# Kernel optimization log

Hardware: AMD Instinct MI355X
Metric: run time of the kernel (lower is better)

## Reference

```python
import jax, jax.numpy as jnp
import numpy as np

N, M, FEAT, GROUP, EMB = 512, 4096, 1024, 16, 64
DIM_GROUP = FEAT // GROUP  # 64


def _make_boxes(key, n):
    k1, k2, k3, k4 = jax.random.split(key, 4)
    cx = jax.random.uniform(k1, (n,), minval=0.0, maxval=800.0)
    cy = jax.random.uniform(k2, (n,), minval=0.0, maxval=800.0)
    w = jax.random.uniform(k3, (n,), minval=16.0, maxval=256.0)
    h = jax.random.uniform(k4, (n,), minval=16.0, maxval=256.0)
    return jnp.stack([cx - 0.5 * w, cy - 0.5 * h, cx + 0.5 * w, cy + 0.5 * h], axis=1)


def setup_inputs() -> dict:
    key = jax.random.key(0)
    ks = jax.random.split(key, 10)
    return {
        "roi_feat": jax.random.normal(ks[0], (N, FEAT), dtype=jnp.float32),
        "ref_feat": jax.random.normal(ks[1], (M, FEAT), dtype=jnp.float32),
        "rois_cur": _make_boxes(ks[2], N),
        "rois_ref": _make_boxes(ks[3], M),
        "Wg_w": jax.random.normal(ks[4], (GROUP, EMB), dtype=jnp.float32) * 0.01,
        "Wg_b": jnp.zeros((GROUP,), dtype=jnp.float32),
        "Wq_w": jax.random.normal(ks[5], (FEAT, FEAT), dtype=jnp.float32) * (1.0 / np.sqrt(FEAT)),
        "Wq_b": jnp.zeros((FEAT,), dtype=jnp.float32),
        "Wk_w": jax.random.normal(ks[6], (FEAT, FEAT), dtype=jnp.float32) * (1.0 / np.sqrt(FEAT)),
        "Wk_b": jnp.zeros((FEAT,), dtype=jnp.float32),
        "Wv_w": jax.random.normal(ks[7], (FEAT, FEAT), dtype=jnp.float32) * 0.01,  # grouped 1x1 conv: [16 groups x 64 out, 1024 in-per-group]
        "Wv_b": jnp.zeros((FEAT,), dtype=jnp.float32),
    }


def _position_embedding(bbox, ref_bbox):
    # extract_position_matrix
    xmin, ymin, xmax, ymax = [ref_bbox[:, i] for i in range(4)]
    w_ref = xmax - xmin + 1.0
    h_ref = ymax - ymin + 1.0
    cx_ref = 0.5 * (xmin + xmax)
    cy_ref = 0.5 * (ymin + ymax)
    xmin, ymin, xmax, ymax = [bbox[:, i] for i in range(4)]
    w = xmax - xmin + 1.0
    h = ymax - ymin + 1.0
    cx = 0.5 * (xmin + xmax)
    cy = 0.5 * (ymin + ymax)
    dx = jnp.log(jnp.abs((cx[:, None] - cx_ref[None, :]) / w[:, None]) + 0.001)
    dy = jnp.log(jnp.abs((cy[:, None] - cy_ref[None, :]) / h[:, None]) + 0.001)
    dw = jnp.log(w[:, None] / w_ref[None, :])
    dh = jnp.log(h[:, None] / h_ref[None, :])
    pos = jnp.stack([dx, dy, dw, dh], axis=2)  # [N, M, 4]
    # extract_position_embedding with feat_dim=64, wave_length=1000
    feat_range = jnp.arange(EMB // 8, dtype=jnp.float32)  # 8
    dim_mat = jnp.power(1000.0, (8.0 / EMB) * feat_range)  # [8]
    div = (pos * 100.0)[..., None] / dim_mat  # [N, M, 4, 8]
    emb = jnp.concatenate([jnp.sin(div), jnp.cos(div)], axis=3)  # [N, M, 4, 16]
    return emb.reshape(pos.shape[0], pos.shape[1], EMB)  # [N, M, 64]


def reference(roi_feat, ref_feat, rois_cur, rois_ref,
              Wg_w, Wg_b, Wq_w, Wq_b, Wk_w, Wk_b, Wv_w, Wv_b):
    emb = _position_embedding(rois_cur, rois_ref)  # [N, M, 64]
    # Wg: 1x1 conv over embedding channels -> per-group bias [N, G, M]
    aff_weight = jax.nn.relu(jnp.einsum('nme,ge->ngm', emb, Wg_w) + Wg_b[None, :, None])
    q = (roi_feat @ Wq_w.T + Wq_b).reshape(-1, GROUP, DIM_GROUP)  # [N, G, dg]
    k = (ref_feat @ Wk_w.T + Wk_b).reshape(-1, GROUP, DIM_GROUP)  # [M, G, dg]
    aff_scale = jnp.einsum('ngd,mgd->ngm', q, k) * (1.0 / np.sqrt(DIM_GROUP))
    weighted_aff = jnp.log(aff_weight + 1e-6) + aff_scale
    aff_softmax = jax.nn.softmax(weighted_aff, axis=2)  # [N, G, M]
    out_t = jnp.einsum('ngm,mf->ngf', aff_softmax, ref_feat)  # [N, G, FEAT]
    # grouped 1x1 conv Wv: group g maps its FEAT inputs to DIM_GROUP outputs
    Wv_g = Wv_w.reshape(GROUP, DIM_GROUP, FEAT)
    output = jnp.einsum('ngf,gof->ngo', out_t, Wv_g).reshape(-1, FEAT) + Wv_b
    return output
```

## Files before the change

kernel.cpp:

```cpp
#include <hip/hip_runtime.h>
#include <hip/hip_bf16.h>

#define N_ROI 512
#define M_REF 4096
#define FEAT 1024
#define GROUP 16
#define DG 64
#define EMB 64
#define GLDH 72
#define MSPLIT 32
#define MRANGE (M_REF / MSPLIT)
#define MCHUNK 64
#define BP2 72
#define PTP 40
#define DEFER_THR 8.0f

using f16x8 = __attribute__((ext_vector_type(8))) _Float16;
using f16x4 = __attribute__((ext_vector_type(4))) _Float16;
using f32x4 = __attribute__((ext_vector_type(4))) float;

__global__ __launch_bounds__(256) void cast_f16_5(
    const float* __restrict__ s0, _Float16* __restrict__ d0, int n0,
    const float* __restrict__ s1, _Float16* __restrict__ d1, int n1,
    const float* __restrict__ s2, _Float16* __restrict__ d2, int n2,
    const float* __restrict__ s3, _Float16* __restrict__ d3, int n3,
    const float* __restrict__ s4, _Float16* __restrict__ d4, int n4) {
  const int q0 = n0 >> 2, q1 = n1 >> 2, q2 = n2 >> 2, q3 = n3 >> 2, q4 = n4 >> 2;
  const int total = q0 + q1 + q2 + q3 + q4;
  for (int i = blockIdx.x * 256 + threadIdx.x; i < total;
       i += gridDim.x * 256) {
    int j = i;
    const float* s;
    _Float16* d;
    if (j < q0) { s = s0; d = d0; }
    else { j -= q0;
      if (j < q1) { s = s1; d = d1; }
      else { j -= q1;
        if (j < q2) { s = s2; d = d2; }
        else { j -= q2;
          if (j < q3) { s = s3; d = d3; }
          else { j -= q3; s = s4; d = d4; } } } }
    float4 v = *(const float4*)&s[(size_t)j * 4];
    *(f16x4*)&d[(size_t)j * 4] =
        f16x4{(_Float16)v.x, (_Float16)v.y, (_Float16)v.z, (_Float16)v.w};
  }
}

__global__ __launch_bounds__(256) void gemm_ff16(
    const _Float16* __restrict__ A, const _Float16* __restrict__ B,
    const float* __restrict__ bias, _Float16* __restrict__ C,
    int M, int N, int K) {
  __shared__ _Float16 As[128 * GLDH];
  __shared__ _Float16 Bs[64 * GLDH];
  const int tid = threadIdx.x, lane = tid & 63, wid = tid >> 6;
  const int bm = blockIdx.y * 128, bn = blockIdx.x * 64;
  const int wr = (wid >> 1) * 64, wc = (wid & 1) * 32;
  const int lrow = lane & 15, lk = (lane >> 4) * 8;

  f16x8 ra[4], rb[2];
#pragma unroll
  for (int i = 0; i < 4; ++i) {
    int idx = tid + i * 256, r = idx >> 3, c = (idx & 7) * 8;
    ra[i] = *(const f16x8*)&A[(size_t)(bm + r) * K + c];
  }
#pragma unroll
  for (int i = 0; i < 2; ++i) {
    int idx = tid + i * 256, r = idx >> 3, c = (idx & 7) * 8;
    rb[i] = *(const f16x8*)&B[(size_t)(bn + r) * K + c];
  }

  f32x4 acc[4][2] = {};
  for (int k0 = 0; k0 < K; k0 += 64) {
#pragma unroll
    for (int i = 0; i < 4; ++i) {
      int idx = tid + i * 256, r = idx >> 3, c = (idx & 7) * 8;
      *(f16x8*)&As[r * GLDH + c] = ra[i];
    }
#pragma unroll
    for (int i = 0; i < 2; ++i) {
      int idx = tid + i * 256, r = idx >> 3, c = (idx & 7) * 8;
      *(f16x8*)&Bs[r * GLDH + c] = rb[i];
    }
    __syncthreads();
    if (k0 + 64 < K) {
#pragma unroll
      for (int i = 0; i < 4; ++i) {
        int idx = tid + i * 256, r = idx >> 3, c = (idx & 7) * 8;
        ra[i] = *(const f16x8*)&A[(size_t)(bm + r) * K + k0 + 64 + c];
      }
#pragma unroll
      for (int i = 0; i < 2; ++i) {
        int idx = tid + i * 256, r = idx >> 3, c = (idx & 7) * 8;
        rb[i] = *(const f16x8*)&B[(size_t)(bn + r) * K + k0 + 64 + c];
      }
    }
    f16x8 a[4][2], b[2][2];
#pragma unroll
    for (int mi = 0; mi < 4; ++mi)
#pragma unroll
      for (int ks = 0; ks < 2; ++ks)
        a[mi][ks] = *(const f16x8*)&As[(wr + mi * 16 + lrow) * GLDH + ks * 32 + lk];
#pragma unroll
    for (int ni = 0; ni < 2; ++ni)
#pragma unroll
      for (int ks = 0; ks < 2; ++ks)
        b[ni][ks] = *(const f16x8*)&Bs[(wc + ni * 16 + lrow) * GLDH + ks * 32 + lk];
#pragma unroll
    for (int ks = 0; ks < 2; ++ks)
#pragma unroll
      for (int mi = 0; mi < 4; ++mi)
#pragma unroll
        for (int ni = 0; ni < 2; ++ni)
          acc[mi][ni] = __builtin_amdgcn_mfma_f32_16x16x32_f16(
              a[mi][ks], b[ni][ks], acc[mi][ni], 0, 0, 0);
    __syncthreads();
  }
#pragma unroll
  for (int mi = 0; mi < 4; ++mi)
#pragma unroll
    for (int ni = 0; ni < 2; ++ni) {
      int col = bn + wc + ni * 16 + lrow;
      float bv = bias ? bias[col] : 0.0f;
#pragma unroll
      for (int i = 0; i < 4; ++i) {
        int row = bm + wr + mi * 16 + (lane >> 4) * 4 + i;
        C[(size_t)row * N + col] = (_Float16)(acc[mi][ni][i] + bv);
      }
    }
}

__global__ __launch_bounds__(512) void attn_fused_kernel(
    const float* __restrict__ rois_cur, const float* __restrict__ rois_ref,
    const float* __restrict__ Wg_w, const float* __restrict__ Wg_b,
    const _Float16* __restrict__ q, const _Float16* __restrict__ k,
    const _Float16* __restrict__ vt, float* __restrict__ pacc,
    float* __restrict__ pml) {
  __shared__ _Float16 Bias[GROUP][16][BP2];
  __shared__ _Float16 pt[8][16][PTP];
  const int tid = threadIdx.x, lane = tid & 63, w = tid >> 6;
  const int bid = blockIdx.x;
  const int split = bid & (MSPLIT - 1), nt = bid >> 5;
  const int n0 = nt * 16;
  const int mb0 = split * MRANGE;
  const int lm = lane & 15, lc = lane >> 4;
  const int g0 = w * 2;
  const int mq = w & 3;
  const int nh = (w >> 2) * 8;

  f16x8 wgf[2];
#pragma unroll
  for (int kc = 0; kc < 2; ++kc) {
    const float* p = Wg_w + lm * EMB + kc * 32 + lc * 8;
#pragma unroll
    for (int j = 0; j < 8; ++j) wgf[kc][j] = (_Float16)p[j];
  }
  float wgb[4];
#pragma unroll
  for (int i = 0; i < 4; ++i) wgb[i] = Wg_b[lc * 4 + i];

  f16x8 qb[2][2];
#pragma unroll
  for (int gi = 0; gi < 2; ++gi)
#pragma unroll
    for (int kc = 0; kc < 2; ++kc)
      qb[gi][kc] = *(const f16x8*)
          &q[(size_t)(n0 + lm) * FEAT + (g0 + gi) * DG + kc * 32 + lc * 8];

  f32x4 acc[2][4] = {};
  float mrun[2] = {-1e30f, -1e30f}, lrun[2] = {0.0f, 0.0f};

  const float inv_dim[8] = {1.0f,          0.42169651f,  0.17782794f,
                            0.074989417f,  0.031622776f, 0.013335214f,
                            0.0056234133f, 0.0023713737f};
  const int isY = lc >> 1;
  const int useCos = lc & 1;

  for (int ch = 0; ch < MRANGE / MCHUNK; ++ch) {
    const int cb = mb0 + ch * MCHUNK;
    const int mglob = cb + mq * 16 + lm;

    const float4 rb = reinterpret_cast<const float4*>(rois_ref)[mglob];
    const float wr_ = rb.z - rb.x + 1.0f, hr_ = rb.w - rb.y + 1.0f;
    const float cxr = 0.5f * (rb.x + rb.z), cyr = 0.5f * (rb.y + rb.w);
    const float lwr = __logf(wr_), lhr = __logf(hr_);

    __syncthreads();

    for (int nl = nh; nl < nh + 8; ++nl) {
      const int n = n0 + nl;
      const float x0 = rois_cur[n * 4 + 0], y0 = rois_cur[n * 4 + 1];
      const float x1 = rois_cur[n * 4 + 2], y1 = rois_cur[n * 4 + 3];
      const float ww = x1 - x0 + 1.0f, hh = y1 - y0 + 1.0f;
      const float cx = 0.5f * (x0 + x1), cy = 0.5f * (y0 + y1);
      float pa, pb;
      if (isY) {
        pa = __logf(fabsf((cy - cyr) / hh) + 0.001f);
        pb = __logf(hh) - lhr;
      } else {
        pa = __logf(fabsf((cx - cxr) / ww) + 0.001f);
        pb = __logf(ww) - lwr;
      }
      pa *= 100.0f;
      pb *= 100.0f;
      f16x8 ef0, ef1;
#pragma unroll
      for (int f = 0; f < 8; ++f) {
        const float xa = pa * inv_dim[f];
        const float xb = pb * inv_dim[f];
        ef0[f] = (_Float16)(useCos ? __cosf(xa) : __sinf(xa));
        ef1[f] = (_Float16)(useCos ? __cosf(xb) : __sinf(xb));
      }
      f32x4 bacc = {};
      bacc = __builtin_amdgcn_mfma_f32_16x16x32_f16(wgf[0], ef0, bacc, 0, 0, 0);
      bacc = __builtin_amdgcn_mfma_f32_16x16x32_f16(wgf[1], ef1, bacc, 0, 0, 0);
#pragma unroll
      for (int i = 0; i < 4; ++i) {
        float v = fmaxf(bacc[i] + wgb[i], 0.0f);
        Bias[lc * 4 + i][nl][mq * 16 + lm] = (_Float16)__logf(v + 1e-6f);
      }
    }
    __syncthreads();

    for (int st = 0; st < 2; ++st) {
      const int ms = cb + st * 32;
#pragma unroll
      for (int gi = 0; gi < 2; ++gi) {
        const int g = g0 + gi;
        const size_t kbase = (size_t)(ms + lm) * FEAT + g * DG + lc * 8;
        f16x8 ka0a = *(const f16x8*)&k[kbase];
        f16x8 ka0b = *(const f16x8*)&k[kbase + 32];
        f16x8 ka1a = *(const f16x8*)&k[kbase + (size_t)16 * FEAT];
        f16x8 ka1b = *(const f16x8*)&k[kbase + (size_t)16 * FEAT + 32];
        f32x4 sAa = {}, sBa = {};
        sAa = __builtin_amdgcn_mfma_f32_16x16x32_f16(ka0a, qb[gi][0], sAa, 0, 0, 0);
        sAa = __builtin_amdgcn_mfma_f32_16x16x32_f16(ka0b, qb[gi][1], sAa, 0, 0, 0);
        sBa = __builtin_amdgcn_mfma_f32_16x16x32_f16(ka1a, qb[gi][0], sBa, 0, 0, 0);
        sBa = __builtin_amdgcn_mfma_f32_16x16x32_f16(ka1b, qb[gi][1], sBa, 0, 0, 0);
        const f16x4 bA = *(const f16x4*)&Bias[g][lm][st * 32 + lc * 4];
        const f16x4 bB = *(const f16x4*)&Bias[g][lm][st * 32 + 16 + lc * 4];
        float s[8];
#pragma unroll
        for (int i = 0; i < 4; ++i) {
          s[i] = (float)bA[i] + sAa[i] * 0.125f;
          s[4 + i] = (float)bB[i] + sBa[i] * 0.125f;
        }
        float cmax = s[0];
#pragma unroll
        for (int i = 1; i < 8; ++i) cmax = fmaxf(cmax, s[i]);
        cmax = fmaxf(cmax, __shfl_xor(cmax, 16));
        cmax = fmaxf(cmax, __shfl_xor(cmax, 32));
        if (!__all(cmax <= mrun[gi] + DEFER_THR)) {
          const float mnew = fmaxf(mrun[gi], cmax);
          const float fac = __expf(mrun[gi] - mnew);
          lrun[gi] *= fac;
          float fr[4];
#pragma unroll
          for (int i = 0; i < 4; ++i) fr[i] = __shfl(fac, lc * 4 + i);
#pragma unroll
          for (int ct = 0; ct < 4; ++ct)
#pragma unroll
            for (int i = 0; i < 4; ++i) acc[gi][ct][i] *= fr[i];
          mrun[gi] = mnew;
        }
        float p[8];
        float csum = 0.0f;
#pragma unroll
        for (int i = 0; i < 8; ++i) {
          p[i] = __expf(s[i] - mrun[gi]);
          csum += p[i];
        }
        csum += __shfl_xor(csum, 16);
        csum += __shfl_xor(csum, 32);
        lrun[gi] += csum;
        f16x4 pA = {(_Float16)p[0], (_Float16)p[1], (_Float16)p[2], (_Float16)p[3]};
        f16x4 pB = {(_Float16)p[4], (_Float16)p[5], (_Float16)p[6], (_Float16)p[7]};
        *(f16x4*)&pt[w][lm][lc * 4] = pA;
        *(f16x4*)&pt[w][lm][16 + lc * 4] = pB;
        const f16x8 pfrag = *(const f16x8*)&pt[w][lm][lc * 8];
#pragma unroll
        for (int ct = 0; ct < 4; ++ct) {
          const f16x8 vf = *(const f16x8*)
              &vt[(size_t)(g * DG + ct * 16 + lm) * M_REF + ms + lc * 8];
          acc[gi][ct] = __builtin_amdgcn_mfma_f32_16x16x32_f16(pfrag, vf,
                                                              acc[gi][ct], 0, 0, 0);
        }
      }
    }
  }

#pragma unroll
  for (int gi = 0; gi < 2; ++gi) {
    const size_t base = (size_t)(nt * GROUP + g0 + gi) * MSPLIT + split;
#pragma unroll
    for (int ct = 0; ct < 4; ++ct)
#pragma unroll
      for (int i = 0; i < 4; ++i)
        pacc[(base * 16 + lc * 4 + i) * 64 + ct * 16 + lm] = acc[gi][ct][i];
    if (lc == 0) {
      pml[(base * 16 + lm) * 2 + 0] = mrun[gi];
      pml[(base * 16 + lm) * 2 + 1] = lrun[gi];
    }
  }
}

__global__ __launch_bounds__(256) void combine_kernel(
    const float* __restrict__ pacc, const float* __restrict__ pml,
    const float* __restrict__ Wv_b, float* __restrict__ out) {
  const int nt = blockIdx.x >> 4, g = blockIdx.x & 15;
  const int r = threadIdx.x >> 4, c0 = (threadIdx.x & 15) * 4;
  const size_t gb = (size_t)(nt * GROUP + g) * MSPLIT;

  float ms[MSPLIT], ls[MSPLIT];
  float M = -1e30f;
#pragma unroll
  for (int s = 0; s < MSPLIT; ++s) {
    ms[s] = pml[((gb + s) * 16 + r) * 2 + 0];
    ls[s] = pml[((gb + s) * 16 + r) * 2 + 1];
    M = fmaxf(M, ms[s]);
  }
  const float inv_base = 1.0f;
  float D = 0.0f;
  float4 o = {0.0f, 0.0f, 0.0f, 0.0f};
  float* po = &o.x;
#pragma unroll
  for (int s = 0; s < MSPLIT; ++s) {
    const float e = __expf(ms[s] - M);
    D += e * ls[s];
    const float4 a = *(const float4*)&pacc[((gb + s) * 16 + r) * 64 + c0];
    po[0] += e * a.x;
    po[1] += e * a.y;
    po[2] += e * a.z;
    po[3] += e * a.w;
  }
  const float inv = inv_base / D;
#pragma unroll
  for (int j = 0; j < 4; ++j)
    po[j] = po[j] * inv + Wv_b[g * DG + c0 + j];
  *(float4*)&out[(size_t)(nt * 16 + r) * FEAT + g * DG + c0] = o;
}

extern "C" void kernel_launch(void* const* d_in, const int* in_sizes, int n_in,
                              void* d_out, int out_size, void* d_ws,
                              size_t ws_size, hipStream_t stream) {
  const float* roi_feat = (const float*)d_in[0];
  const float* ref_feat = (const float*)d_in[1];
  const float* rois_cur = (const float*)d_in[2];
  const float* rois_ref = (const float*)d_in[3];
  const float* Wg_w = (const float*)d_in[4];
  const float* Wg_b = (const float*)d_in[5];
  const float* Wq_w = (const float*)d_in[6];
  const float* Wq_b = (const float*)d_in[7];
  const float* Wk_w = (const float*)d_in[8];
  const float* Wk_b = (const float*)d_in[9];
  const float* Wv_w = (const float*)d_in[10];
  const float* Wv_b = (const float*)d_in[11];
  float* out = (float*)d_out;

  _Float16* q16 = (_Float16*)d_ws;
  _Float16* k16 = q16 + (size_t)N_ROI * FEAT;
  _Float16* vt16 = k16 + (size_t)M_REF * FEAT;
  _Float16* roi16 = vt16 + (size_t)FEAT * M_REF;
  _Float16* ref16 = roi16 + (size_t)N_ROI * FEAT;
  _Float16* wq16 = ref16 + (size_t)M_REF * FEAT;
  _Float16* wk16 = wq16 + (size_t)FEAT * FEAT;
  _Float16* wv16 = wk16 + (size_t)FEAT * FEAT;
  float* pacc = (float*)(wv16 + (size_t)FEAT * FEAT);
  float* pml = pacc + (size_t)N_ROI * GROUP * MSPLIT * 64;

  cast_f16_5<<<dim3(2048), 256, 0, stream>>>(
      roi_feat, roi16, N_ROI * FEAT, ref_feat, ref16, M_REF * FEAT,
      Wq_w, wq16, FEAT * FEAT, Wk_w, wk16, FEAT * FEAT,
      Wv_w, wv16, FEAT * FEAT);

  gemm_ff16<<<dim3(FEAT / 64, N_ROI / 128), 256, 0, stream>>>(
      roi16, wq16, Wq_b, q16, N_ROI, FEAT, FEAT);
  gemm_ff16<<<dim3(FEAT / 64, M_REF / 128), 256, 0, stream>>>(
      ref16, wk16, Wk_b, k16, M_REF, FEAT, FEAT);
  gemm_ff16<<<dim3(M_REF / 64, FEAT / 128), 256, 0, stream>>>(
      wv16, ref16, nullptr, vt16, FEAT, M_REF, FEAT);

  attn_fused_kernel<<<dim3((N_ROI / 16) * MSPLIT), 512, 0, stream>>>(
      rois_cur, rois_ref, Wg_w, Wg_b, q16, k16, vt16, pacc, pml);

  combine_kernel<<<dim3((N_ROI / 16) * GROUP), 256, 0, stream>>>(
      pacc, pml, Wv_b, out);
}
```

Before: 259.7 us.

## Transpose PV MFMA to drop LDS P round-trip and store fp16 partials

The P·V product is computed with swapped operands (V as A, P as B), so the softmax probabilities in registers already match the B-fragment layout. This removes the per-wave shared-memory staging of P, and lets the rescale factor apply per lane without shuffles. Partial accumulators are written as fp16 in a row-contiguous layout, which halves partial-sum traffic into the combine kernel. Launch bounds now request higher occupancy. The costs are fp16 rounding of the split partials and extra register pressure from the occupancy hint.

```diff
diff --git a/kernel.cpp b/kernel.cpp
--- a/kernel.cpp
+++ b/kernel.cpp
@@ -12,7 +12,6 @@
 #define MRANGE (M_REF / MSPLIT)
 #define MCHUNK 64
 #define BP2 72
-#define PTP 40
 #define DEFER_THR 8.0f
 
 using f16x8 = __attribute__((ext_vector_type(8))) _Float16;
@@ -129,14 +128,13 @@
     }
 }
 
-__global__ __launch_bounds__(512) void attn_fused_kernel(
+__global__ __launch_bounds__(512, 8) void attn_fused_kernel(
     const float* __restrict__ rois_cur, const float* __restrict__ rois_ref,
     const float* __restrict__ Wg_w, const float* __restrict__ Wg_b,
     const _Float16* __restrict__ q, const _Float16* __restrict__ k,
-    const _Float16* __restrict__ vt, float* __restrict__ pacc,
+    const _Float16* __restrict__ vt, _Float16* __restrict__ pacc,
     float* __restrict__ pml) {
   __shared__ _Float16 Bias[GROUP][16][BP2];
-  __shared__ _Float16 pt[8][16][PTP];
   const int tid = threadIdx.x, lane = tid & 63, w = tid >> 6;
   const int bid = blockIdx.x;
   const int split = bid & (MSPLIT - 1), nt = bid >> 5;
@@ -253,13 +251,10 @@
           const float mnew = fmaxf(mrun[gi], cmax);
           const float fac = __expf(mrun[gi] - mnew);
           lrun[gi] *= fac;
-          float fr[4];
-#pragma unroll
-          for (int i = 0; i < 4; ++i) fr[i] = __shfl(fac, lc * 4 + i);
 #pragma unroll
           for (int ct = 0; ct < 4; ++ct)
 #pragma unroll
-            for (int i = 0; i < 4; ++i) acc[gi][ct][i] *= fr[i];
+            for (int i = 0; i < 4; ++i) acc[gi][ct][i] *= fac;
           mrun[gi] = mnew;
         }
         float p[8];
@@ -272,16 +267,17 @@
         csum += __shfl_xor(csum, 16);
         csum += __shfl_xor(csum, 32);
         lrun[gi] += csum;
-        f16x4 pA = {(_Float16)p[0], (_Float16)p[1], (_Float16)p[2], (_Float16)p[3]};
-        f16x4 pB = {(_Float16)p[4], (_Float16)p[5], (_Float16)p[6], (_Float16)p[7]};
-        *(f16x4*)&pt[w][lm][lc * 4] = pA;
-        *(f16x4*)&pt[w][lm][16 + lc * 4] = pB;
-        const f16x8 pfrag = *(const f16x8*)&pt[w][lm][lc * 8];
+        f16x8 pfrag;
+#pragma unroll
+        for (int j = 0; j < 8; ++j) pfrag[j] = (_Float16)p[j];
 #pragma unroll
         for (int ct = 0; ct < 4; ++ct) {
-          const f16x8 vf = *(const f16x8*)
-              &vt[(size_t)(g * DG + ct * 16 + lm) * M_REF + ms + lc * 8];
-          acc[gi][ct] = __builtin_amdgcn_mfma_f32_16x16x32_f16(pfrag, vf,
+          const size_t vrow = (size_t)(g * DG + ct * 16 + lm) * M_REF + ms;
+          const f16x4 vA = *(const f16x4*)&vt[vrow + lc * 4];
+          const f16x4 vB = *(const f16x4*)&vt[vrow + 16 + lc * 4];
+          const f16x8 vf = {vA[0], vA[1], vA[2], vA[3],
+                            vB[0], vB[1], vB[2], vB[3]};
+          acc[gi][ct] = __builtin_amdgcn_mfma_f32_16x16x32_f16(vf, pfrag,
                                                               acc[gi][ct], 0, 0, 0);
         }
       }
@@ -292,10 +288,11 @@
   for (int gi = 0; gi < 2; ++gi) {
     const size_t base = (size_t)(nt * GROUP + g0 + gi) * MSPLIT + split;
 #pragma unroll
-    for (int ct = 0; ct < 4; ++ct)
-#pragma unroll
-      for (int i = 0; i < 4; ++i)
-        pacc[(base * 16 + lc * 4 + i) * 64 + ct * 16 + lm] = acc[gi][ct][i];
+    for (int ct = 0; ct < 4; ++ct) {
+      f16x4 h = {(_Float16)acc[gi][ct][0], (_Float16)acc[gi][ct][1],
+                 (_Float16)acc[gi][ct][2], (_Float16)acc[gi][ct][3]};
+      *(f16x4*)&pacc[(base * 16 + lm) * 64 + ct * 16 + lc * 4] = h;
+    }
     if (lc == 0) {
       pml[(base * 16 + lm) * 2 + 0] = mrun[gi];
       pml[(base * 16 + lm) * 2 + 1] = lrun[gi];
@@ -304,35 +301,33 @@
 }
 
 __global__ __launch_bounds__(256) void combine_kernel(
-    const float* __restrict__ pacc, const float* __restrict__ pml,
+    const _Float16* __restrict__ pacc, const float* __restrict__ pml,
     const float* __restrict__ Wv_b, float* __restrict__ out) {
   const int nt = blockIdx.x >> 4, g = blockIdx.x & 15;
   const int r = threadIdx.x >> 4, c0 = (threadIdx.x & 15) * 4;
   const size_t gb = (size_t)(nt * GROUP + g) * MSPLIT;
 
-  float ms[MSPLIT], ls[MSPLIT];
+  float ms[MSPLIT];
   float M = -1e30f;
 #pragma unroll
   for (int s = 0; s < MSPLIT; ++s) {
     ms[s] = pml[((gb + s) * 16 + r) * 2 + 0];
-    ls[s] = pml[((gb + s) * 16 + r) * 2 + 1];
     M = fmaxf(M, ms[s]);
   }
-  const float inv_base = 1.0f;
   float D = 0.0f;
   float4 o = {0.0f, 0.0f, 0.0f, 0.0f};
   float* po = &o.x;
 #pragma unroll
   for (int s = 0; s < MSPLIT; ++s) {
     const float e = __expf(ms[s] - M);
-    D += e * ls[s];
-    const float4 a = *(const float4*)&pacc[((gb + s) * 16 + r) * 64 + c0];
-    po[0] += e * a.x;
-    po[1] += e * a.y;
-    po[2] += e * a.z;
-    po[3] += e * a.w;
-  }
-  const float inv = inv_base / D;
+    D += e * pml[((gb + s) * 16 + r) * 2 + 1];
+    const f16x4 a = *(const f16x4*)&pacc[((gb + s) * 16 + r) * 64 + c0];
+    po[0] += e * (float)a[0];
+    po[1] += e * (float)a[1];
+    po[2] += e * (float)a[2];
+    po[3] += e * (float)a[3];
+  }
+  const float inv = 1.0f / D;
 #pragma unroll
   for (int j = 0; j < 4; ++j)
     po[j] = po[j] * inv + Wv_b[g * DG + c0 + j];
@@ -364,8 +359,8 @@
   _Float16* wq16 = ref16 + (size_t)M_REF * FEAT;
   _Float16* wk16 = wq16 + (size_t)FEAT * FEAT;
   _Float16* wv16 = wk16 + (size_t)FEAT * FEAT;
-  float* pacc = (float*)(wv16 + (size_t)FEAT * FEAT);
-  float* pml = pacc + (size_t)N_ROI * GROUP * MSPLIT * 64;
+  _Float16* pacc = wv16 + (size_t)FEAT * FEAT;
+  float* pml = (float*)(pacc + (size_t)N_ROI * GROUP * MSPLIT * 64);
 
   cast_f16_5<<<dim3(2048), 256, 0, stream>>>(
       roi_feat, roi16, N_ROI * FEAT, ref_feat, ref16, M_REF * FEAT,
```

Result: slower. 324.7 us (+25.0%).
